# Optimization experiments

Hardware: AMD Instinct MI355X
Metric: run time of the kernel (lower is better)

## Reference

```python
import jax, jax.numpy as jnp
import numpy as np

N_NODES = 100000
SELF_LOOP_W = 2.0  # improved=True in PyG GCNConv -> self-loop fill value 2.0


def gcn_conv(x, src, dst, ew, W, b, n_nodes):
    """PyG GCNConv (improved=True): x' = D^-1/2 (A + 2I) D^-1/2 (x W) + b."""
    h = x @ W  # [N, out]
    loop = jnp.arange(n_nodes, dtype=src.dtype)
    src_f = jnp.concatenate([src, loop])
    dst_f = jnp.concatenate([dst, loop])
    ew_f = jnp.concatenate([ew, jnp.full((n_nodes,), SELF_LOOP_W, dtype=ew.dtype)])
    deg = jax.ops.segment_sum(ew_f, dst_f, num_segments=n_nodes)  # [N]
    dinv = jnp.where(deg > 0, jax.lax.rsqrt(jnp.where(deg > 0, deg, 1.0)), 0.0)
    norm = dinv[src_f] * ew_f * dinv[dst_f]  # [E+N]
    msg = h[src_f] * norm[:, None]  # [E+N, out]
    out = jax.ops.segment_sum(msg, dst_f, num_segments=n_nodes)
    return out + b


def setup_inputs() -> dict:
    key = jax.random.key(0)
    k1, k2, k3, k4, k5 = jax.random.split(key, 5)
    N, E = N_NODES, 3200000
    F0, F1, F2 = 128, 128, 64
    x = jax.random.normal(k1, (N, F0), dtype=jnp.float32)
    edges = jax.random.randint(k2, (2, E), 0, N, dtype=jnp.int64)
    weights = jax.random.uniform(k3, (E,), dtype=jnp.float32)
    # kaiming_uniform on weight of shape [out, in]; stored transposed for x @ W
    bnd0 = float(np.sqrt(6.0 / F0))
    bnd1 = float(np.sqrt(6.0 / F1))
    W0 = jax.random.uniform(k4, (F0, F1), dtype=jnp.float32, minval=-bnd0, maxval=bnd0)
    W1 = jax.random.uniform(k5, (F1, F2), dtype=jnp.float32, minval=-bnd1, maxval=bnd1)
    b0 = jnp.zeros((F1,), dtype=jnp.float32)
    b1 = jnp.zeros((F2,), dtype=jnp.float32)
    return {"x": x, "edges": edges, "weights": weights,
            "W0": W0, "b0": b0, "W1": W1, "b1": b1}


def reference(x, edges, weights, W0, b0, W1, b1):
    src, dst = edges[0], edges[1]
    n = x.shape[0]
    h = gcn_conv(x, src, dst, weights, W0, b0, n)
    h = jax.nn.relu(h)
    h = gcn_conv(h, src, dst, weights, W1, b1, n)
    return jax.nn.sigmoid(h)
```

## Files before the change

### kernel.cpp

```cpp
#include <hip/hip_runtime.h>
#include <math.h>

typedef __attribute__((ext_vector_type(8))) short bf16x8;
typedef __attribute__((ext_vector_type(4))) float f32x4;


__device__ __forceinline__ unsigned short f2b(float f) {
  unsigned u = __float_as_uint(f);
  unsigned r = u + 0x7fffu + ((u >> 16) & 1u);
  return (unsigned short)(r >> 16);
}
__device__ __forceinline__ float b2f_lo(unsigned v) {
  return __uint_as_float(v << 16);
}
__device__ __forceinline__ float b2f_hi(unsigned v) {
  return __uint_as_float(v & 0xffff0000u);
}


__global__ __launch_bounds__(256) void bucket_hist(const int* __restrict__ dst,
                                                   int* __restrict__ blkhist,
                                                   int NB, int E, int chunk) {
  extern __shared__ int sm_hist[];
  for (int i = threadIdx.x; i < NB; i += 256) sm_hist[i] = 0;
  __syncthreads();
  const int b = blockIdx.x;
  const int beg = b * chunk;
  const int end = min(E, beg + chunk);
  for (int j = beg + threadIdx.x; j < end; j += 256)
    atomicAdd(&sm_hist[dst[j] >> 6], 1);
  __syncthreads();
  for (int i = threadIdx.x; i < NB; i += 256) blkhist[(long)b * NB + i] = sm_hist[i];
}

__global__ __launch_bounds__(256) void col_prefix(int* __restrict__ blkhist,
                                                  int* __restrict__ btot, int NB,
                                                  int nblk) {
  const int k = blockIdx.x * 256 + threadIdx.x;
  if (k >= NB) return;
  int run = 0;
  int b = 0;
  for (; b + 4 <= nblk; b += 4) {
    const int t0 = blkhist[(long)(b + 0) * NB + k];
    const int t1 = blkhist[(long)(b + 1) * NB + k];
    const int t2 = blkhist[(long)(b + 2) * NB + k];
    const int t3 = blkhist[(long)(b + 3) * NB + k];
    blkhist[(long)(b + 0) * NB + k] = run; run += t0;
    blkhist[(long)(b + 1) * NB + k] = run; run += t1;
    blkhist[(long)(b + 2) * NB + k] = run; run += t2;
    blkhist[(long)(b + 3) * NB + k] = run; run += t3;
  }
  for (; b < nblk; ++b) {
    const int t = blkhist[(long)b * NB + k];
    blkhist[(long)b * NB + k] = run;
    run += t;
  }
  btot[k] = run;
}


__global__ __launch_bounds__(256) void scan_bsum(const int* __restrict__ count,
                                                 int* __restrict__ bsum, int N) {
  __shared__ int sm[256];
  int i = blockIdx.x * 256 + threadIdx.x;
  sm[threadIdx.x] = (i < N) ? count[i] : 0;
  __syncthreads();
  for (int off = 128; off > 0; off >>= 1) {
    if (threadIdx.x < off) sm[threadIdx.x] += sm[threadIdx.x + off];
    __syncthreads();
  }
  if (threadIdx.x == 0) bsum[blockIdx.x] = sm[0];
}

__global__ __launch_bounds__(512) void scan_bscan(int* __restrict__ bsum, int nblk) {
  __shared__ int sm[512];
  int t = threadIdx.x;
  int v = (t < nblk) ? bsum[t] : 0;
  sm[t] = v;
  __syncthreads();
  for (int off = 1; off < 512; off <<= 1) {
    int a = (t >= off) ? sm[t - off] : 0;
    __syncthreads();
    sm[t] += a;
    __syncthreads();
  }
  if (t < nblk) bsum[t] = sm[t] - v;
}

__global__ __launch_bounds__(256) void scan_inplace(int* __restrict__ cr,
                                                    const int* __restrict__ bscan,
                                                    int N) {
  __shared__ int sm[256];
  int i = blockIdx.x * 256 + threadIdx.x;
  int t = threadIdx.x;
  int v = (i < N) ? cr[i] : 0;
  sm[t] = v;
  __syncthreads();
  for (int off = 1; off < 256; off <<= 1) {
    int a = (t >= off) ? sm[t - off] : 0;
    __syncthreads();
    sm[t] += a;
    __syncthreads();
  }
  int excl = sm[t] - v + bscan[blockIdx.x];
  if (i < N) cr[i] = excl;
  if (i == N - 1) cr[N] = excl + v;
}

__global__ __launch_bounds__(256) void bucket_scatter(const int* __restrict__ src,
                                                      const int* __restrict__ dst,
                                                      const float* __restrict__ ew,
                                                      const int* __restrict__ blkhist,
                                                      const int* __restrict__ bstart,
                                                      uint2* __restrict__ bkt, int NB,
                                                      int E, int chunk) {
  extern __shared__ int sm_cur[];
  const int b = blockIdx.x;
  for (int i = threadIdx.x; i < NB; i += 256)
    sm_cur[i] = blkhist[(long)b * NB + i] + bstart[i];
  __syncthreads();
  const int beg = b * chunk;
  const int end = min(E, beg + chunk);
  for (int j = beg + threadIdx.x; j < end; j += 256) {
    const int d = dst[j];
    int q = (int)(ew[j] * 32767.f + 0.5f);
    q = (q < 0) ? 0 : ((q > 32767) ? 32767 : q);
    const unsigned rec = ((unsigned)src[j] << 15) | (unsigned)q;
    const int pos = atomicAdd(&sm_cur[d >> 6], 1);
    bkt[pos] = make_uint2(rec, (unsigned)(d & 63));
  }
}

__global__ __launch_bounds__(256) void bucket_finalize(const uint2* __restrict__ bkt,
                                                       const int* __restrict__ bstart,
                                                       unsigned* __restrict__ recs,
                                                       int* __restrict__ row_start,
                                                       float* __restrict__ dinv, int NB,
                                                       int N, int E) {
  __shared__ int hist[64], qs[64], cur[64], lstart[64];
  const int k = blockIdx.x;
  const int t = threadIdx.x;
  if (t < 64) { hist[t] = 0; qs[t] = 0; }
  __syncthreads();
  const int beg = bstart[k], end = bstart[k + 1];
  for (int j = beg + t; j < end; j += 256) {
    const uint2 v = bkt[j];
    atomicAdd(&hist[v.y], 1);
    atomicAdd(&qs[v.y], (int)(v.x & 32767u));
  }
  __syncthreads();
  if (t == 0) {
    int run = 0;
    for (int i = 0; i < 64; ++i) { lstart[i] = run; run += hist[i]; }
  }
  __syncthreads();
  if (t < 64) {
    cur[t] = lstart[t];
    const int node = k * 64 + t;
    if (node < N) {
      row_start[node] = beg + lstart[t];
      dinv[node] = rsqrtf((float)qs[t] * (1.f / 32767.f) + 2.0f);
    }
  }
  if (k == NB - 1 && t == 0) row_start[N] = E;
  __syncthreads();
  for (int j = beg + t; j < end; j += 256) {
    const uint2 v = bkt[j];
    const int off = atomicAdd(&cur[v.y], 1);
    recs[beg + off] = v.x;
  }
}


__global__ __launch_bounds__(256) void fold_dinv(unsigned int* __restrict__ recs,
                                                 const float* __restrict__ dinv, int E) {
  int i = blockIdx.x * 256 + threadIdx.x;
  if (i >= E) return;
  const unsigned rec = recs[i];
  const int s = rec >> 15;
  const float v = (float)(rec & 32767u) * (1.f / 32767.f) * dinv[s];
  int q = (int)(v * (32767.f / 0.75f) + 0.5f);
  q = (q > 32767) ? 32767 : q;
  recs[i] = ((unsigned)s << 15) | (unsigned)q;
}


__global__ __launch_bounds__(256) void to_bf16_8(const float* __restrict__ x,
                                                 unsigned short* __restrict__ xb,
                                                 int n8) {
  int i = blockIdx.x * 256 + threadIdx.x;
  if (i >= n8) return;
  const float4 a = *(const float4*)&x[(long)i * 8];
  const float4 b = *(const float4*)&x[(long)i * 8 + 4];
  uint4 o;
  o.x = (unsigned)f2b(a.x) | ((unsigned)f2b(a.y) << 16);
  o.y = (unsigned)f2b(a.z) | ((unsigned)f2b(a.w) << 16);
  o.z = (unsigned)f2b(b.x) | ((unsigned)f2b(b.y) << 16);
  o.w = (unsigned)f2b(b.z) | ((unsigned)f2b(b.w) << 16);
  *(uint4*)&xb[(long)i * 8] = o;
}

__global__ __launch_bounds__(256) void pack_wfrag(const float* __restrict__ W,
                                                  unsigned short* __restrict__ frag,
                                                  int C, int total) {
  int i = blockIdx.x * 256 + threadIdx.x;
  if (i >= total) return;
  const int e = i & 7;
  const int lane = (i >> 3) & 63;
  const int t = i >> 9;
  const int kk = t & 3;
  const int ct = t >> 2;
  const int k = kk * 32 + (lane >> 4) * 8 + e;
  const int c = ct * 16 + (lane & 15);
  frag[i] = f2b(W[(long)k * C + c]);
}


__global__ __launch_bounds__(256) void gather_l1(const uint4* __restrict__ xb4,
                                                 const unsigned int* __restrict__ recs,
                                                 const int* __restrict__ row_start,
                                                 const float* __restrict__ dinv,
                                                 uint4* __restrict__ xab4, int N) {
  const int t = blockIdx.x * 256 + threadIdx.x;
  const int d = t >> 4;
  if (d >= N) return;
  const int jl = t & 15;
  const int beg = row_start[d], end = row_start[d + 1];
  const float dd = dinv[d];
  constexpr float S = 0.75f / 32767.f;
  const uint4 sv = xb4[(long)d * 16 + jl];
  const float sl = 2.f * dd * dd;
  float aca[8], acb[8];
  aca[0] = b2f_lo(sv.x) * sl; aca[1] = b2f_hi(sv.x) * sl;
  aca[2] = b2f_lo(sv.y) * sl; aca[3] = b2f_hi(sv.y) * sl;
  aca[4] = b2f_lo(sv.z) * sl; aca[5] = b2f_hi(sv.z) * sl;
  aca[6] = b2f_lo(sv.w) * sl; aca[7] = b2f_hi(sv.w) * sl;
#pragma unroll
  for (int u = 0; u < 8; ++u) acb[u] = 0.f;
  int j = beg;
  for (; j + 8 <= end; j += 8) {
    unsigned rr[8];
    uint4 vv[8];
#pragma unroll
    for (int u = 0; u < 8; ++u) rr[u] = recs[j + u];
#pragma unroll
    for (int u = 0; u < 8; ++u) vv[u] = xb4[(long)(rr[u] >> 15) * 16 + jl];
#pragma unroll
    for (int u = 0; u < 8; ++u) {
      const float cf = (float)(rr[u] & 32767u) * S * dd;
      if (u & 1) {
        acb[0] = fmaf(cf, b2f_lo(vv[u].x), acb[0]);
        acb[1] = fmaf(cf, b2f_hi(vv[u].x), acb[1]);
        acb[2] = fmaf(cf, b2f_lo(vv[u].y), acb[2]);
        acb[3] = fmaf(cf, b2f_hi(vv[u].y), acb[3]);
        acb[4] = fmaf(cf, b2f_lo(vv[u].z), acb[4]);
        acb[5] = fmaf(cf, b2f_hi(vv[u].z), acb[5]);
        acb[6] = fmaf(cf, b2f_lo(vv[u].w), acb[6]);
        acb[7] = fmaf(cf, b2f_hi(vv[u].w), acb[7]);
      } else {
        aca[0] = fmaf(cf, b2f_lo(vv[u].x), aca[0]);
        aca[1] = fmaf(cf, b2f_hi(vv[u].x), aca[1]);
        aca[2] = fmaf(cf, b2f_lo(vv[u].y), aca[2]);
        aca[3] = fmaf(cf, b2f_hi(vv[u].y), aca[3]);
        aca[4] = fmaf(cf, b2f_lo(vv[u].z), aca[4]);
        aca[5] = fmaf(cf, b2f_hi(vv[u].z), aca[5]);
        aca[6] = fmaf(cf, b2f_lo(vv[u].w), aca[6]);
        aca[7] = fmaf(cf, b2f_hi(vv[u].w), aca[7]);
      }
    }
  }
  for (; j < end; ++j) {
    const unsigned rec = recs[j];
    const uint4 v = xb4[(long)(rec >> 15) * 16 + jl];
    const float cf = (float)(rec & 32767u) * S * dd;
    aca[0] = fmaf(cf, b2f_lo(v.x), aca[0]);
    aca[1] = fmaf(cf, b2f_hi(v.x), aca[1]);
    aca[2] = fmaf(cf, b2f_lo(v.y), aca[2]);
    aca[3] = fmaf(cf, b2f_hi(v.y), aca[3]);
    aca[4] = fmaf(cf, b2f_lo(v.z), aca[4]);
    aca[5] = fmaf(cf, b2f_hi(v.z), aca[5]);
    aca[6] = fmaf(cf, b2f_lo(v.w), aca[6]);
    aca[7] = fmaf(cf, b2f_hi(v.w), aca[7]);
  }
#pragma unroll
  for (int u = 0; u < 8; ++u) aca[u] += acb[u];
  uint4 o;
  o.x = (unsigned)f2b(aca[0]) | ((unsigned)f2b(aca[1]) << 16);
  o.y = (unsigned)f2b(aca[2]) | ((unsigned)f2b(aca[3]) << 16);
  o.z = (unsigned)f2b(aca[4]) | ((unsigned)f2b(aca[5]) << 16);
  o.w = (unsigned)f2b(aca[6]) | ((unsigned)f2b(aca[7]) << 16);
  xab4[(long)d * 16 + jl] = o;
}


__global__ __launch_bounds__(256) void fused_mlp_mfma(
    const unsigned short* __restrict__ xab, const unsigned short* __restrict__ w0f,
    const float* __restrict__ b0, const unsigned short* __restrict__ w1f,
    unsigned short* __restrict__ r2b, int N) {
  __shared__ unsigned short Hl[4][16][136];
  const int tid = threadIdx.x;
  const int w = tid >> 6, l = tid & 63;
  const int lr = l & 15, lg = l >> 4;
  const int row0 = blockIdx.x * 64 + w * 16;

  int arow = row0 + lr;
  if (arow >= N) arow = N - 1;
  const unsigned short* ap = xab + (long)arow * 128 + lg * 8;
  const bf16x8 a0 = *(const bf16x8*)(ap);
  const bf16x8 a1 = *(const bf16x8*)(ap + 32);
  const bf16x8 a2 = *(const bf16x8*)(ap + 64);
  const bf16x8 a3 = *(const bf16x8*)(ap + 96);

  for (int ct = 0; ct < 8; ++ct) {
    const unsigned short* bp = w0f + ct * 2048 + l * 8;
    f32x4 acc = {0.f, 0.f, 0.f, 0.f};
    acc = __builtin_amdgcn_mfma_f32_16x16x32_bf16(a0, *(const bf16x8*)(bp), acc, 0, 0, 0);
    acc = __builtin_amdgcn_mfma_f32_16x16x32_bf16(a1, *(const bf16x8*)(bp + 512), acc, 0, 0, 0);
    acc = __builtin_amdgcn_mfma_f32_16x16x32_bf16(a2, *(const bf16x8*)(bp + 1024), acc, 0, 0, 0);
    acc = __builtin_amdgcn_mfma_f32_16x16x32_bf16(a3, *(const bf16x8*)(bp + 1536), acc, 0, 0, 0);
    const float bv = b0[ct * 16 + lr];
#pragma unroll
    for (int r = 0; r < 4; ++r) {
      Hl[w][lg * 4 + r][ct * 16 + lr] = f2b(fmaxf(acc[r] + bv, 0.f));
    }
  }

  const unsigned short* hp = &Hl[w][lr][lg * 8];
  const bf16x8 h0 = *(const bf16x8*)(hp);
  const bf16x8 h1 = *(const bf16x8*)(hp + 32);
  const bf16x8 h2 = *(const bf16x8*)(hp + 64);
  const bf16x8 h3 = *(const bf16x8*)(hp + 96);

  for (int ct = 0; ct < 4; ++ct) {
    const unsigned short* bp = w1f + ct * 2048 + l * 8;
    f32x4 acc = {0.f, 0.f, 0.f, 0.f};
    acc = __builtin_amdgcn_mfma_f32_16x16x32_bf16(h0, *(const bf16x8*)(bp), acc, 0, 0, 0);
    acc = __builtin_amdgcn_mfma_f32_16x16x32_bf16(h1, *(const bf16x8*)(bp + 512), acc, 0, 0, 0);
    acc = __builtin_amdgcn_mfma_f32_16x16x32_bf16(h2, *(const bf16x8*)(bp + 1024), acc, 0, 0, 0);
    acc = __builtin_amdgcn_mfma_f32_16x16x32_bf16(h3, *(const bf16x8*)(bp + 1536), acc, 0, 0, 0);
#pragma unroll
    for (int r = 0; r < 4; ++r) {
      const int orow = row0 + lg * 4 + r;
      if (orow < N) r2b[(long)orow * 64 + ct * 16 + lr] = f2b(acc[r]);
    }
  }
}


__global__ __launch_bounds__(256) void gather_l2(const uint4* __restrict__ r2b4,
                                                 const unsigned int* __restrict__ recs,
                                                 const int* __restrict__ row_start,
                                                 const float* __restrict__ dinv,
                                                 const float* __restrict__ b1,
                                                 float* __restrict__ out, int N) {
  const int t = blockIdx.x * 256 + threadIdx.x;
  const int d = t >> 3;
  if (d >= N) return;
  const int jl = t & 7;
  const int beg = row_start[d], end = row_start[d + 1];
  const float dd = dinv[d];
  constexpr float S = 0.75f / 32767.f;
  const uint4 sv = r2b4[(long)d * 8 + jl];
  const float sl = 2.f * dd * dd;
  float aca[8], acb[8];
  aca[0] = b2f_lo(sv.x) * sl; aca[1] = b2f_hi(sv.x) * sl;
  aca[2] = b2f_lo(sv.y) * sl; aca[3] = b2f_hi(sv.y) * sl;
  aca[4] = b2f_lo(sv.z) * sl; aca[5] = b2f_hi(sv.z) * sl;
  aca[6] = b2f_lo(sv.w) * sl; aca[7] = b2f_hi(sv.w) * sl;
#pragma unroll
  for (int u = 0; u < 8; ++u) acb[u] = 0.f;
  int j = beg;
  for (; j + 8 <= end; j += 8) {
    unsigned rr[8];
    uint4 vv[8];
#pragma unroll
    for (int u = 0; u < 8; ++u) rr[u] = recs[j + u];
#pragma unroll
    for (int u = 0; u < 8; ++u) vv[u] = r2b4[(long)(rr[u] >> 15) * 8 + jl];
#pragma unroll
    for (int u = 0; u < 8; ++u) {
      const float cf = (float)(rr[u] & 32767u) * S * dd;
      if (u & 1) {
        acb[0] = fmaf(cf, b2f_lo(vv[u].x), acb[0]);
        acb[1] = fmaf(cf, b2f_hi(vv[u].x), acb[1]);
        acb[2] = fmaf(cf, b2f_lo(vv[u].y), acb[2]);
        acb[3] = fmaf(cf, b2f_hi(vv[u].y), acb[3]);
        acb[4] = fmaf(cf, b2f_lo(vv[u].z), acb[4]);
        acb[5] = fmaf(cf, b2f_hi(vv[u].z), acb[5]);
        acb[6] = fmaf(cf, b2f_lo(vv[u].w), acb[6]);
        acb[7] = fmaf(cf, b2f_hi(vv[u].w), acb[7]);
      } else {
        aca[0] = fmaf(cf, b2f_lo(vv[u].x), aca[0]);
        aca[1] = fmaf(cf, b2f_hi(vv[u].x), aca[1]);
        aca[2] = fmaf(cf, b2f_lo(vv[u].y), aca[2]);
        aca[3] = fmaf(cf, b2f_hi(vv[u].y), aca[3]);
        aca[4] = fmaf(cf, b2f_lo(vv[u].z), aca[4]);
        aca[5] = fmaf(cf, b2f_hi(vv[u].z), aca[5]);
        aca[6] = fmaf(cf, b2f_lo(vv[u].w), aca[6]);
        aca[7] = fmaf(cf, b2f_hi(vv[u].w), aca[7]);
      }
    }
  }
  for (; j < end; ++j) {
    const unsigned rec = recs[j];
    const uint4 v = r2b4[(long)(rec >> 15) * 8 + jl];
    const float cf = (float)(rec & 32767u) * S * dd;
    aca[0] = fmaf(cf, b2f_lo(v.x), aca[0]);
    aca[1] = fmaf(cf, b2f_hi(v.x), aca[1]);
    aca[2] = fmaf(cf, b2f_lo(v.y), aca[2]);
    aca[3] = fmaf(cf, b2f_hi(v.y), aca[3]);
    aca[4] = fmaf(cf, b2f_lo(v.z), aca[4]);
    aca[5] = fmaf(cf, b2f_hi(v.z), aca[5]);
    aca[6] = fmaf(cf, b2f_lo(v.w), aca[6]);
    aca[7] = fmaf(cf, b2f_hi(v.w), aca[7]);
  }
#pragma unroll
  for (int u = 0; u < 8; ++u) aca[u] += acb[u];
  const int c = jl * 8;
  const float4 ba = *(const float4*)&b1[c];
  const float4 bb = *(const float4*)&b1[c + 4];
  float4 o1, o2;
  o1.x = 1.f / (1.f + __expf(-(aca[0] + ba.x)));
  o1.y = 1.f / (1.f + __expf(-(aca[1] + ba.y)));
  o1.z = 1.f / (1.f + __expf(-(aca[2] + ba.z)));
  o1.w = 1.f / (1.f + __expf(-(aca[3] + ba.w)));
  o2.x = 1.f / (1.f + __expf(-(aca[4] + bb.x)));
  o2.y = 1.f / (1.f + __expf(-(aca[5] + bb.y)));
  o2.z = 1.f / (1.f + __expf(-(aca[6] + bb.z)));
  o2.w = 1.f / (1.f + __expf(-(aca[7] + bb.w)));
  *(float4*)&out[(long)d * 64 + c] = o1;
  *(float4*)&out[(long)d * 64 + c + 4] = o2;
}


extern "C" void kernel_launch(void* const* d_in, const int* in_sizes, int n_in,
                              void* d_out, int out_size, void* d_ws, size_t ws_size,
                              hipStream_t stream) {
  const float* x  = (const float*)d_in[0];
  const int* src  = (const int*)d_in[1];
  const float* ew = (const float*)d_in[2];
  const float* W0 = (const float*)d_in[3];
  const float* b0 = (const float*)d_in[4];
  const float* W1 = (const float*)d_in[5];
  const float* b1 = (const float*)d_in[6];
  float* out = (float*)d_out;

  const int N = in_sizes[0] / 128;
  const int E = in_sizes[2];
  const int* dstp = src + E;

  const int NB = (N + 63) >> 6;
  const int NBLK = 256;
  const int chunk = (E + NBLK - 1) / NBLK;

  float* ws = (float*)d_ws;
  const size_t oN = ((size_t)N + 255) & ~(size_t)255;
  float* dinv = ws;
  int* rowst = (int*)(ws + oN);
  int* bstart = rowst + oN;
  int* bsum = bstart + 2048;
  int* blkhist = bsum + 1024;
  unsigned int* recs = (unsigned int*)(blkhist + (size_t)NBLK * NB);
  unsigned int* xb = recs + E;
  uint2* bkt = (uint2*)xb;
  const size_t xb_units = ((size_t)2 * E > (size_t)N * 64) ? (size_t)2 * E : (size_t)N * 64;
  unsigned int* xab = xb + xb_units;
  unsigned short* w0f = (unsigned short*)(xab + (size_t)N * 64);
  unsigned short* w1f = w0f + 16384;
  unsigned int* r2b = xb;

  const int nbE = (E + 255) / 256;
  const int nblkB = (NB + 255) / 256;

  bucket_hist<<<NBLK, 256, NB * 4, stream>>>(dstp, blkhist, NB, E, chunk);
  col_prefix<<<nblkB, 256, 0, stream>>>(blkhist, bstart, NB, NBLK);
  scan_bsum<<<nblkB, 256, 0, stream>>>(bstart, bsum, NB);
  scan_bscan<<<1, 512, 0, stream>>>(bsum, nblkB);
  scan_inplace<<<nblkB, 256, 0, stream>>>(bstart, bsum, NB);
  bucket_scatter<<<NBLK, 256, NB * 4, stream>>>(src, dstp, ew, blkhist, bstart, bkt, NB,
                                                E, chunk);
  bucket_finalize<<<NB, 256, 0, stream>>>(bkt, bstart, recs, rowst, dinv, NB, N, E);
  fold_dinv<<<nbE, 256, 0, stream>>>(recs, dinv, E);

  pack_wfrag<<<64, 256, 0, stream>>>(W0, w0f, 128, 16384);
  pack_wfrag<<<32, 256, 0, stream>>>(W1, w1f, 64, 8192);
  to_bf16_8<<<(N * 16 + 255) / 256, 256, 0, stream>>>(x, (unsigned short*)xb, N * 16);

  gather_l1<<<(N * 16 + 255) / 256, 256, 0, stream>>>((const uint4*)xb, recs, rowst, dinv,
                                                      (uint4*)xab, N);
  fused_mlp_mfma<<<(N + 63) / 64, 256, 0, stream>>>((const unsigned short*)xab, w0f, b0,
                                                    w1f, (unsigned short*)r2b, N);
  gather_l2<<<(N * 8 + 255) / 256, 256, 0, stream>>>((const uint4*)r2b, recs, rowst, dinv,
                                                     b1, out, N);
}
```

Before: 326.3 us.

## Split layer-1 gather into two feature-half passes and merge scan kernels

The layer-1 gather now runs as two launches, each covering half of the 128 feature columns (8 lanes per node instead of 16). The working set of gathered rows per pass is halved (128 B per row instead of 256 B), which is meant to fit better in L2/MALL and improve hit rates on random source-row reads. The cost is reading the CSR records and row pointers twice. Separately, the three-kernel bucket prefix scan is replaced by a single-block looping scan, removing two launches at the price of serialising the scan in one workgroup.

```diff
diff --git a/kernel.cpp b/kernel.cpp
--- a/kernel.cpp
+++ b/kernel.cpp
@@ -58,53 +58,30 @@
   btot[k] = run;
 }
 
-
-__global__ __launch_bounds__(256) void scan_bsum(const int* __restrict__ count,
-                                                 int* __restrict__ bsum, int N) {
+__global__ __launch_bounds__(256) void scan_single(int* __restrict__ cr, int n) {
   __shared__ int sm[256];
-  int i = blockIdx.x * 256 + threadIdx.x;
-  sm[threadIdx.x] = (i < N) ? count[i] : 0;
-  __syncthreads();
-  for (int off = 128; off > 0; off >>= 1) {
-    if (threadIdx.x < off) sm[threadIdx.x] += sm[threadIdx.x + off];
+  __shared__ int sbase;
+  if (threadIdx.x == 0) sbase = 0;
+  __syncthreads();
+  for (int c0 = 0; c0 < n; c0 += 256) {
+    const int i = c0 + threadIdx.x;
+    const int v = (i < n) ? cr[i] : 0;
+    sm[threadIdx.x] = v;
     __syncthreads();
-  }
-  if (threadIdx.x == 0) bsum[blockIdx.x] = sm[0];
-}
-
-__global__ __launch_bounds__(512) void scan_bscan(int* __restrict__ bsum, int nblk) {
-  __shared__ int sm[512];
-  int t = threadIdx.x;
-  int v = (t < nblk) ? bsum[t] : 0;
-  sm[t] = v;
-  __syncthreads();
-  for (int off = 1; off < 512; off <<= 1) {
-    int a = (t >= off) ? sm[t - off] : 0;
+    for (int off = 1; off < 256; off <<= 1) {
+      int a = (threadIdx.x >= off) ? sm[threadIdx.x - off] : 0;
+      __syncthreads();
+      sm[threadIdx.x] += a;
+      __syncthreads();
+    }
+    const int b = sbase;
+    const int tot = sm[255];
+    if (i < n) cr[i] = b + sm[threadIdx.x] - v;
     __syncthreads();
-    sm[t] += a;
+    if (threadIdx.x == 0) sbase = b + tot;
     __syncthreads();
   }
-  if (t < nblk) bsum[t] = sm[t] - v;
-}
-
-__global__ __launch_bounds__(256) void scan_inplace(int* __restrict__ cr,
-                                                    const int* __restrict__ bscan,
-                                                    int N) {
-  __shared__ int sm[256];
-  int i = blockIdx.x * 256 + threadIdx.x;
-  int t = threadIdx.x;
-  int v = (i < N) ? cr[i] : 0;
-  sm[t] = v;
-  __syncthreads();
-  for (int off = 1; off < 256; off <<= 1) {
-    int a = (t >= off) ? sm[t - off] : 0;
-    __syncthreads();
-    sm[t] += a;
-    __syncthreads();
-  }
-  int excl = sm[t] - v + bscan[blockIdx.x];
-  if (i < N) cr[i] = excl;
-  if (i == N - 1) cr[N] = excl + v;
+  if (threadIdx.x == 0) cr[n] = sbase;
 }
 
 __global__ __launch_bounds__(256) void bucket_scatter(const int* __restrict__ src,
@@ -216,15 +193,16 @@
 }
 
 
-__global__ __launch_bounds__(256) void gather_l1(const uint4* __restrict__ xb4,
-                                                 const unsigned int* __restrict__ recs,
-                                                 const int* __restrict__ row_start,
-                                                 const float* __restrict__ dinv,
-                                                 uint4* __restrict__ xab4, int N) {
+__global__ __launch_bounds__(256) void gather_l1_half(const uint4* __restrict__ xb4,
+                                                      const unsigned int* __restrict__ recs,
+                                                      const int* __restrict__ row_start,
+                                                      const float* __restrict__ dinv,
+                                                      uint4* __restrict__ xab4, int N,
+                                                      int half) {
   const int t = blockIdx.x * 256 + threadIdx.x;
-  const int d = t >> 4;
+  const int d = t >> 3;
   if (d >= N) return;
-  const int jl = t & 15;
+  const int jl = (t & 7) + half * 8;
   const int beg = row_start[d], end = row_start[d + 1];
   const float dd = dinv[d];
   constexpr float S = 0.75f / 32767.f;
@@ -248,25 +226,15 @@
 #pragma unroll
     for (int u = 0; u < 8; ++u) {
       const float cf = (float)(rr[u] & 32767u) * S * dd;
-      if (u & 1) {
-        acb[0] = fmaf(cf, b2f_lo(vv[u].x), acb[0]);
-        acb[1] = fmaf(cf, b2f_hi(vv[u].x), acb[1]);
-        acb[2] = fmaf(cf, b2f_lo(vv[u].y), acb[2]);
-        acb[3] = fmaf(cf, b2f_hi(vv[u].y), acb[3]);
-        acb[4] = fmaf(cf, b2f_lo(vv[u].z), acb[4]);
-        acb[5] = fmaf(cf, b2f_hi(vv[u].z), acb[5]);
-        acb[6] = fmaf(cf, b2f_lo(vv[u].w), acb[6]);
-        acb[7] = fmaf(cf, b2f_hi(vv[u].w), acb[7]);
-      } else {
-        aca[0] = fmaf(cf, b2f_lo(vv[u].x), aca[0]);
-        aca[1] = fmaf(cf, b2f_hi(vv[u].x), aca[1]);
-        aca[2] = fmaf(cf, b2f_lo(vv[u].y), aca[2]);
-        aca[3] = fmaf(cf, b2f_hi(vv[u].y), aca[3]);
-        aca[4] = fmaf(cf, b2f_lo(vv[u].z), aca[4]);
-        aca[5] = fmaf(cf, b2f_hi(vv[u].z), aca[5]);
-        aca[6] = fmaf(cf, b2f_lo(vv[u].w), aca[6]);
-        aca[7] = fmaf(cf, b2f_hi(vv[u].w), aca[7]);
-      }
+      float* ac = (u & 1) ? acb : aca;
+      ac[0] = fmaf(cf, b2f_lo(vv[u].x), ac[0]);
+      ac[1] = fmaf(cf, b2f_hi(vv[u].x), ac[1]);
+      ac[2] = fmaf(cf, b2f_lo(vv[u].y), ac[2]);
+      ac[3] = fmaf(cf, b2f_hi(vv[u].y), ac[3]);
+      ac[4] = fmaf(cf, b2f_lo(vv[u].z), ac[4]);
+      ac[5] = fmaf(cf, b2f_hi(vv[u].z), ac[5]);
+      ac[6] = fmaf(cf, b2f_lo(vv[u].w), ac[6]);
+      ac[7] = fmaf(cf, b2f_hi(vv[u].w), ac[7]);
     }
   }
   for (; j < end; ++j) {
@@ -380,25 +348,15 @@
 #pragma unroll
     for (int u = 0; u < 8; ++u) {
       const float cf = (float)(rr[u] & 32767u) * S * dd;
-      if (u & 1) {
-        acb[0] = fmaf(cf, b2f_lo(vv[u].x), acb[0]);
-        acb[1] = fmaf(cf, b2f_hi(vv[u].x), acb[1]);
-        acb[2] = fmaf(cf, b2f_lo(vv[u].y), acb[2]);
-        acb[3] = fmaf(cf, b2f_hi(vv[u].y), acb[3]);
-        acb[4] = fmaf(cf, b2f_lo(vv[u].z), acb[4]);
-        acb[5] = fmaf(cf, b2f_hi(vv[u].z), acb[5]);
-        acb[6] = fmaf(cf, b2f_lo(vv[u].w), acb[6]);
-        acb[7] = fmaf(cf, b2f_hi(vv[u].w), acb[7]);
-      } else {
-        aca[0] = fmaf(cf, b2f_lo(vv[u].x), aca[0]);
-        aca[1] = fmaf(cf, b2f_hi(vv[u].x), aca[1]);
-        aca[2] = fmaf(cf, b2f_lo(vv[u].y), aca[2]);
-        aca[3] = fmaf(cf, b2f_hi(vv[u].y), aca[3]);
-        aca[4] = fmaf(cf, b2f_lo(vv[u].z), aca[4]);
-        aca[5] = fmaf(cf, b2f_hi(vv[u].z), aca[5]);
-        aca[6] = fmaf(cf, b2f_lo(vv[u].w), aca[6]);
-        aca[7] = fmaf(cf, b2f_hi(vv[u].w), aca[7]);
-      }
+      float* ac = (u & 1) ? acb : aca;
+      ac[0] = fmaf(cf, b2f_lo(vv[u].x), ac[0]);
+      ac[1] = fmaf(cf, b2f_hi(vv[u].x), ac[1]);
+      ac[2] = fmaf(cf, b2f_lo(vv[u].y), ac[2]);
+      ac[3] = fmaf(cf, b2f_hi(vv[u].y), ac[3]);
+      ac[4] = fmaf(cf, b2f_lo(vv[u].z), ac[4]);
+      ac[5] = fmaf(cf, b2f_hi(vv[u].z), ac[5]);
+      ac[6] = fmaf(cf, b2f_lo(vv[u].w), ac[6]);
+      ac[7] = fmaf(cf, b2f_hi(vv[u].w), ac[7]);
     }
   }
   for (; j < end; ++j) {
@@ -474,9 +432,7 @@
 
   bucket_hist<<<NBLK, 256, NB * 4, stream>>>(dstp, blkhist, NB, E, chunk);
   col_prefix<<<nblkB, 256, 0, stream>>>(blkhist, bstart, NB, NBLK);
-  scan_bsum<<<nblkB, 256, 0, stream>>>(bstart, bsum, NB);
-  scan_bscan<<<1, 512, 0, stream>>>(bsum, nblkB);
-  scan_inplace<<<nblkB, 256, 0, stream>>>(bstart, bsum, NB);
+  scan_single<<<1, 256, 0, stream>>>(bstart, NB);
   bucket_scatter<<<NBLK, 256, NB * 4, stream>>>(src, dstp, ew, blkhist, bstart, bkt, NB,
                                                 E, chunk);
   bucket_finalize<<<NB, 256, 0, stream>>>(bkt, bstart, recs, rowst, dinv, NB, N, E);
@@ -486,8 +442,12 @@
   pack_wfrag<<<32, 256, 0, stream>>>(W1, w1f, 64, 8192);
   to_bf16_8<<<(N * 16 + 255) / 256, 256, 0, stream>>>(x, (unsigned short*)xb, N * 16);
 
-  gather_l1<<<(N * 16 + 255) / 256, 256, 0, stream>>>((const uint4*)xb, recs, rowst, dinv,
-                                                      (uint4*)xab, N);
+  const int gl1b = (N * 8 + 255) / 256;
+  gather_l1_half<<<gl1b, 256, 0, stream>>>((const uint4*)xb, recs, rowst, dinv,
+                                           (uint4*)xab, N, 0);
+  gather_l1_half<<<gl1b, 256, 0, stream>>>((const uint4*)xb, recs, rowst, dinv,
+                                           (uint4*)xab, N, 1);
+
   fused_mlp_mfma<<<(N + 63) / 64, 256, 0, stream>>>((const unsigned short*)xab, w0f, b0,
                                                     w1f, (unsigned short*)r2b, N);
   gather_l2<<<(N * 8 + 255) / 256, 256, 0, stream>>>((const uint4*)r2b, recs, rowst, dinv,
```

Measured after the change: 328.8 us. No clear change (+0.8%).
